# Optimization experiments

Hardware: AMD Instinct MI355X
Metric: run time of the kernel (lower is better)

## Reference

```python
import jax, jax.numpy as jnp
import numpy as np

GAMMA = 20
LAMBDA_INV = 25.0


def setup_inputs() -> dict:
    key = jax.random.key(0)
    k1, k2 = jax.random.split(key)
    B, P, D = 128, 512, 384
    z = jax.random.normal(k1, (B, P, D), dtype=jnp.float32)
    view_ids = jax.random.randint(k2, (P,), 0, 2, dtype=jnp.int64)
    return {"z": z, "view_ids": view_ids}


def reference(z, view_ids):
    B, P, D = z.shape
    # [B, P, P] pairwise similarity per image
    sim = jnp.einsum('bpd,bqd->bpq', z, z)
    # valid pairs: different view and not self
    mask_view = view_ids[None, :] != view_ids[:, None]          # [P, P]
    mask = mask_view & ~jnp.eye(P, dtype=bool)
    sim = jnp.where(mask[None, :, :], sim, jnp.float32(-1.0))
    best_sim = sim.max(axis=2)                                   # [B, P]
    best_j = sim.argmax(axis=2)                                  # [B, P]
    # flatten across batch, global top-gamma anchors
    best_sim_flat = best_sim.reshape(-1)                         # [B*P]
    offsets = jnp.arange(B, dtype=best_j.dtype)[:, None] * P
    best_j_flat = (best_j + offsets).reshape(-1)                 # [B*P]
    topk_vals, topk_idx = jax.lax.top_k(best_sim_flat, GAMMA)
    z_flat = z.reshape(-1, D)
    z1 = z_flat[topk_idx]                                        # anchors
    z2 = z_flat[best_j_flat[topk_idx]]                           # matches
    loss = LAMBDA_INV * jnp.mean((z1 - z2) ** 2)
    fmatch_avg_cos = jax.lax.stop_gradient(topk_vals.mean())
    return loss, fmatch_avg_cos
```

## Files before the change

kernel.cpp:

```cpp
#include <hip/hip_runtime.h>


#define NB 128
#define NP 512
#define ND 384
#define NGAMMA 20
#define NKS 12

typedef __attribute__((ext_vector_type(8))) short short8;
typedef __attribute__((ext_vector_type(4))) float f32x4;

__device__ __forceinline__ unsigned short f2bf(float f) {
    unsigned int u = __float_as_uint(f);
    u += 0x7fffu + ((u >> 16) & 1u);
    return (unsigned short)(u >> 16);
}

__device__ __forceinline__ void gload16(const void* gptr, void* lptr) {
    __builtin_amdgcn_global_load_lds(
        (const __attribute__((address_space(1))) void*)gptr,
        (__attribute__((address_space(3))) void*)lptr, 16, 0, 0);
}

__global__ __launch_bounds__(256) void fm_convert(
    const float* __restrict__ z, unsigned short* __restrict__ zhi)
{
    size_t i = (size_t)blockIdx.x * 256 + threadIdx.x;
    const float4* zp = (const float4*)z + i * 2;
    float4 v0 = zp[0], v1 = zp[1];
    float f[8] = {v0.x, v0.y, v0.z, v0.w, v1.x, v1.y, v1.z, v1.w};
    short8 s;
#pragma unroll
    for (int j = 0; j < 8; ++j) s[j] = (short)f2bf(f[j]);
    *(short8*)&zhi[i * 8] = s;
}

__global__ __launch_bounds__(256, 4) void fm_gemm(
    const unsigned short* __restrict__ zhi, const int* __restrict__ view,
    float* __restrict__ pval, int* __restrict__ pidx)
{
    __shared__ __align__(16) unsigned short Ah[2][4][128][8];
    __shared__ __align__(16) unsigned short Bh[2][4][128][8];
    __shared__ int vs[NP];
    __shared__ float lsv[2][2][64];
    __shared__ int   lsi[2][2][64];
    __shared__ float lqv[2][2][64];
    __shared__ int   lqi[2][2][64];

    const int tid  = threadIdx.x;
    const int lane = tid & 63;
    const int wid  = tid >> 6;
    const int wr   = wid >> 1, wc = wid & 1;
    const int g    = lane >> 4, r = lane & 15;

    const int bid  = blockIdx.x;
    const int gidx = (bid & 7) * 160 + (bid >> 3);
    const int b    = gidx / 10;
    const int t    = gidx % 10;
    int tr, tc;
    if (t < 4)      { tr = 0; tc = t; }
    else if (t < 7) { tr = 1; tc = t - 3; }
    else if (t < 9) { tr = 2; tc = t - 5; }
    else            { tr = 3; tc = 3; }
    const bool diag = (tr == tc);
    const int p0 = tr * 128, q0 = tc * 128;

    vs[tid]       = view[tid];
    vs[tid + 256] = view[tid + 256];
    __builtin_amdgcn_sched_barrier(0);

    const size_t zb = (size_t)b * NP * ND;

    f32x4 acc[4][4];
#pragma unroll
    for (int mi = 0; mi < 4; ++mi)
#pragma unroll
        for (int ni = 0; ni < 4; ++ni) acc[mi][ni] = (f32x4){0.f, 0.f, 0.f, 0.f};

#define STAGE(BUF, KT)                                                           \
    do {                                                                         \
        _Pragma("unroll")                                                        \
        for (int i = 0; i < 2; ++i) {                                            \
            const int c_  = wid * 2 + i;                                         \
            const int kg_ = c_ >> 1;                                             \
            const int rb_ = (c_ & 1) * 64;                                       \
            gload16(zhi + zb + (size_t)(p0 + rb_ + lane) * ND + (KT) * 32 + kg_ * 8, \
                    &Ah[BUF][kg_][rb_][0]);                                      \
            if (!diag)                                                           \
                gload16(zhi + zb + (size_t)(q0 + rb_ + lane) * ND + (KT) * 32 + kg_ * 8, \
                        &Bh[BUF][kg_][rb_][0]);                                  \
        }                                                                        \
    } while (0)

#define COMPUTE(BUF)                                                             \
    do {                                                                         \
        short8 ah_[4], bh_[4];                                                   \
        _Pragma("unroll")                                                        \
        for (int mi = 0; mi < 4; ++mi)                                           \
            ah_[mi] = *(const short8*)&Ah[BUF][g][wr * 64 + mi * 16 + r][0];     \
        _Pragma("unroll")                                                        \
        for (int ni = 0; ni < 4; ++ni)                                           \
            bh_[ni] = diag ? *(const short8*)&Ah[BUF][g][wc * 64 + ni * 16 + r][0] \
                           : *(const short8*)&Bh[BUF][g][wc * 64 + ni * 16 + r][0]; \
        _Pragma("unroll")                                                        \
        for (int mi = 0; mi < 4; ++mi)                                           \
            _Pragma("unroll")                                                    \
            for (int ni = 0; ni < 4; ++ni)                                       \
                acc[mi][ni] = __builtin_amdgcn_mfma_f32_16x16x32_bf16(           \
                    ah_[mi], bh_[ni], acc[mi][ni], 0, 0, 0);                     \
    } while (0)

    STAGE(0, 0);
#pragma unroll
    for (int kt = 0; kt < NKS; ++kt) {
        const int cur = kt & 1;
        __builtin_amdgcn_s_barrier();
        __builtin_amdgcn_sched_barrier(0);
        if (kt + 1 < NKS) {
            STAGE(cur ^ 1, kt + 1);
            if (diag) asm volatile("s_waitcnt vmcnt(2)" ::: "memory");
            else      asm volatile("s_waitcnt vmcnt(4)" ::: "memory");
        } else {
            asm volatile("s_waitcnt vmcnt(0)" ::: "memory");
        }
        __builtin_amdgcn_s_barrier();
        __builtin_amdgcn_sched_barrier(0);
        COMPUTE(cur);
    }
#undef STAGE
#undef COMPUTE

#pragma unroll
    for (int mi = 0; mi < 4; ++mi) {
#pragma unroll
        for (int j = 0; j < 4; ++j) {
            const int prow = p0 + wr * 64 + mi * 16 + g * 4 + j;
            const int rv = vs[prow];
            float bv = -2.0f; int bq = 0;
#pragma unroll
            for (int ni = 0; ni < 4; ++ni) {
                const int q = q0 + wc * 64 + ni * 16 + r;
                const float v = (vs[q] != rv) ? acc[mi][ni][j] : -1.0f;
                if (v > bv) { bv = v; bq = q; }
            }
#pragma unroll
            for (int off = 1; off < 16; off <<= 1) {
                const float ov = __shfl_xor(bv, off);
                const int   oq = __shfl_xor(bq, off);
                if (ov > bv || (ov == bv && oq < bq)) { bv = ov; bq = oq; }
            }
            if (r == 0) {
                lsv[wr][wc][mi * 16 + g * 4 + j] = bv;
                lsi[wr][wc][mi * 16 + g * 4 + j] = bq;
            }
        }
    }
    if (!diag) {
#pragma unroll
        for (int ni = 0; ni < 4; ++ni) {
            const int q = q0 + wc * 64 + ni * 16 + r;
            const int qv = vs[q];
            float bv = -2.0f; int bp = 0;
#pragma unroll
            for (int mi = 0; mi < 4; ++mi)
#pragma unroll
                for (int j = 0; j < 4; ++j) {
                    const int prow = p0 + wr * 64 + mi * 16 + g * 4 + j;
                    const float v = (vs[prow] != qv) ? acc[mi][ni][j] : -1.0f;
                    if (v > bv) { bv = v; bp = prow; }
                }
#pragma unroll
            for (int off = 16; off < 64; off <<= 1) {
                const float ov = __shfl_xor(bv, off);
                const int   op = __shfl_xor(bp, off);
                if (ov > bv || (ov == bv && op < bp)) { bv = ov; bp = op; }
            }
            if (g == 0) {
                lqv[wc][wr][ni * 16 + r] = bv;
                lqi[wc][wr][ni * 16 + r] = bp;
            }
        }
    }
    __syncthreads();
    if (tid < 128) {
        const int half = tid >> 6, row = tid & 63;
        {
            float v0 = lsv[half][0][row]; int i0 = lsi[half][0][row];
            const float v1 = lsv[half][1][row]; const int i1 = lsi[half][1][row];
            if (v1 > v0) { v0 = v1; i0 = i1; }
            const int p = p0 + half * 64 + row;
            pval[((size_t)b * NP + p) * 4 + tc] = v0;
            pidx[((size_t)b * NP + p) * 4 + tc] = i0;
        }
        if (!diag) {
            float v0 = lqv[half][0][row]; int i0 = lqi[half][0][row];
            const float v1 = lqv[half][1][row]; const int i1 = lqi[half][1][row];
            if (v1 > v0) { v0 = v1; i0 = i1; }
            const int q = q0 + half * 64 + row;
            pval[((size_t)b * NP + q) * 4 + tr] = v0;
            pidx[((size_t)b * NP + q) * 4 + tr] = i0;
        }
    }
}

__global__ __launch_bounds__(256) void fm_topk_local(
    const float* __restrict__ pval, float* __restrict__ cval, int* __restrict__ cidx)
{
    __shared__ float sv[1024];
    __shared__ float wv[4];
    __shared__ int   wi[4];

    const int t = threadIdx.x;
    const int base = blockIdx.x * 1024;
#pragma unroll
    for (int i = 0; i < 4; ++i) {
        const int e = t + 256 * i;
        const float4 pv = ((const float4*)pval)[base + e];
        float bv = pv.x;
        if (pv.y > bv) bv = pv.y;
        if (pv.z > bv) bv = pv.z;
        if (pv.w > bv) bv = pv.w;
        sv[e] = bv;
    }
    __syncthreads();

    const int lane = t & 63, w = t >> 6;
    for (int it = 0; it < NGAMMA; ++it) {
        float v = sv[t];
        int pos = t;
#pragma unroll
        for (int i = 1; i < 4; ++i) {
            const int e = t + 256 * i;
            const float x = sv[e];
            if (x > v || (x == v && e < pos)) { v = x; pos = e; }
        }
#pragma unroll
        for (int off = 1; off < 64; off <<= 1) {
            const float ov = __shfl_xor(v, off);
            const int   op = __shfl_xor(pos, off);
            if (ov > v || (ov == v && op < pos)) { v = ov; pos = op; }
        }
        if (lane == 0) { wv[w] = v; wi[w] = pos; }
        __syncthreads();
        if (t == 0) {
            float bv2 = wv[0];
            int bp = wi[0];
            for (int k = 1; k < 4; ++k)
                if (wv[k] > bv2 || (wv[k] == bv2 && wi[k] < bp)) { bv2 = wv[k]; bp = wi[k]; }
            cval[blockIdx.x * NGAMMA + it] = bv2;
            cidx[blockIdx.x * NGAMMA + it] = base + bp;
            sv[bp] = -1e30f;
        }
        __syncthreads();
    }
}

__global__ __launch_bounds__(256) void fm_final(
    const float* __restrict__ cval, const int* __restrict__ cidx,
    const float* __restrict__ pval, const int* __restrict__ pidx,
    const float* __restrict__ z, float* __restrict__ out)
{
    __shared__ float sv[1280];
    __shared__ int   si[1280];
    __shared__ float wv[4];
    __shared__ int   wi[4];
    __shared__ int   sel[NGAMMA];
    __shared__ int   selj[NGAMMA];
    __shared__ float ssum;
    __shared__ float red[4];

    const int t = threadIdx.x;
    for (int e = t; e < 1280; e += 256) { sv[e] = cval[e]; si[e] = cidx[e]; }
    if (t == 0) ssum = 0.f;
    __syncthreads();

    const int lane = t & 63, w = t >> 6;
    for (int it = 0; it < NGAMMA; ++it) {
        float v = sv[t];
        int pos = t;
        for (int e = t + 256; e < 1280; e += 256) {
            const float x = sv[e];
            if (x > v || (x == v && e < pos)) { v = x; pos = e; }
        }
#pragma unroll
        for (int off = 1; off < 64; off <<= 1) {
            const float ov = __shfl_xor(v, off);
            const int   op = __shfl_xor(pos, off);
            if (ov > v || (ov == v && op < pos)) { v = ov; pos = op; }
        }
        if (lane == 0) { wv[w] = v; wi[w] = pos; }
        __syncthreads();
        if (t == 0) {
            float bv2 = wv[0];
            int bp = wi[0];
            for (int k = 1; k < 4; ++k)
                if (wv[k] > bv2 || (wv[k] == bv2 && wi[k] < bp)) { bv2 = wv[k]; bp = wi[k]; }
            sel[it] = si[bp];
            ssum += bv2;
            sv[bp] = -1e30f;
        }
        __syncthreads();
    }

    if (t < NGAMMA) {
        const int a = sel[t];
        const float4 pv = ((const float4*)pval)[a];
        float bv = pv.x; int bc = 0;
        if (pv.y > bv) { bv = pv.y; bc = 1; }
        if (pv.z > bv) { bv = pv.z; bc = 2; }
        if (pv.w > bv) { bv = pv.w; bc = 3; }
        selj[t] = ((a >> 9) << 9) + pidx[(size_t)a * 4 + bc];
    }
    __syncthreads();

    float acc = 0.f;
    for (int pr = 0; pr < NGAMMA; ++pr) {
        const int a = sel[pr];
        const int j = selj[pr];
        const float* za = z + (size_t)a * ND;
        const float* zj = z + (size_t)j * ND;
        for (int d = t; d < ND; d += 256) {
            const float df = za[d] - zj[d];
            acc = fmaf(df, df, acc);
        }
    }
#pragma unroll
    for (int off = 1; off < 64; off <<= 1) acc += __shfl_xor(acc, off);
    if (lane == 0) red[w] = acc;
    __syncthreads();
    if (t == 0) {
        const float tot = red[0] + red[1] + red[2] + red[3];
        out[0] = 25.0f * tot / (float)(NGAMMA * ND);
        out[1] = ssum / (float)NGAMMA;
    }
}

extern "C" void kernel_launch(void* const* d_in, const int* in_sizes, int n_in,
                              void* d_out, int out_size, void* d_ws, size_t ws_size,
                              hipStream_t stream)
{
    const float* z    = (const float*)d_in[0];
    const int*   view = (const int*)d_in[1];
    float*       out  = (float*)d_out;
    char* ws = (char*)d_ws;

    const size_t zhi_off  = 0;
    const size_t pval_off = (size_t)NB * NP * ND * 2;
    const size_t pidx_off = pval_off + (size_t)NB * NP * 4 * 4;
    const size_t cval_off = pidx_off + (size_t)NB * NP * 4 * 4;
    const size_t cidx_off = cval_off + 64 * NGAMMA * 4;

    unsigned short* zhi = (unsigned short*)(ws + zhi_off);
    float* pval = (float*)(ws + pval_off);
    int*   pidx = (int*)(ws + pidx_off);
    float* cval = (float*)(ws + cval_off);
    int*   cidx = (int*)(ws + cidx_off);

    fm_convert<<<(NB * NP * ND) / (8 * 256), 256, 0, stream>>>(z, zhi);
    fm_gemm<<<NB * 10, 256, 0, stream>>>(zhi, view, pval, pidx);
    fm_topk_local<<<(NB * NP) / 1024, 256, 0, stream>>>(pval, cval, cidx);
    fm_final<<<1, 256, 0, stream>>>(cval, cidx, pval, pidx, z, out);
}
```

Baseline: 130.5 us.

## Triple-buffer GEMM loads, drop diag special case, use single-wave top-k kernels

The GEMM moves from a double-buffered to a triple-buffered LDS pipeline with two tiles in flight. It needs only one barrier per k-step, and the epilogue scratch arrays now alias the A buffer to save shared memory. Diagonal tiles now also load B instead of reusing A, which adds redundant global traffic for those tiles. Both top-k kernels become single-wavefront register-resident selections that use no shared memory and no block barriers, cutting per-iteration synchronisation. Occupancy hint drops from 4 to 3 blocks per CU.

Result: slower. 147.4 us (+12.9%).

```diff
diff --git a/kernel.cpp b/kernel.cpp
--- a/kernel.cpp
+++ b/kernel.cpp
@@ -35,17 +35,17 @@
     *(short8*)&zhi[i * 8] = s;
 }
 
-__global__ __launch_bounds__(256, 4) void fm_gemm(
+__global__ __launch_bounds__(256, 3) void fm_gemm(
     const unsigned short* __restrict__ zhi, const int* __restrict__ view,
     float* __restrict__ pval, int* __restrict__ pidx)
 {
-    __shared__ __align__(16) unsigned short Ah[2][4][128][8];
-    __shared__ __align__(16) unsigned short Bh[2][4][128][8];
+    __shared__ __align__(16) unsigned short Ah[3][4][128][8];
+    __shared__ __align__(16) unsigned short Bh[3][4][128][8];
     __shared__ int vs[NP];
-    __shared__ float lsv[2][2][64];
-    __shared__ int   lsi[2][2][64];
-    __shared__ float lqv[2][2][64];
-    __shared__ int   lqi[2][2][64];
+    float* lsv = (float*)&Ah[0][0][0][0];
+    int*   lsi = (int*)lsv + 256;
+    float* lqv = (float*)((int*)lsv + 512);
+    int*   lqi = (int*)lsv + 768;
 
     const int tid  = threadIdx.x;
     const int lane = tid & 63;
@@ -86,9 +86,8 @@
             const int rb_ = (c_ & 1) * 64;                                       \
             gload16(zhi + zb + (size_t)(p0 + rb_ + lane) * ND + (KT) * 32 + kg_ * 8, \
                     &Ah[BUF][kg_][rb_][0]);                                      \
-            if (!diag)                                                           \
-                gload16(zhi + zb + (size_t)(q0 + rb_ + lane) * ND + (KT) * 32 + kg_ * 8, \
-                        &Bh[BUF][kg_][rb_][0]);                                  \
+            gload16(zhi + zb + (size_t)(q0 + rb_ + lane) * ND + (KT) * 32 + kg_ * 8, \
+                    &Bh[BUF][kg_][rb_][0]);                                      \
         }                                                                        \
     } while (0)
 
@@ -100,8 +99,7 @@
             ah_[mi] = *(const short8*)&Ah[BUF][g][wr * 64 + mi * 16 + r][0];     \
         _Pragma("unroll")                                                        \
         for (int ni = 0; ni < 4; ++ni)                                           \
-            bh_[ni] = diag ? *(const short8*)&Ah[BUF][g][wc * 64 + ni * 16 + r][0] \
-                           : *(const short8*)&Bh[BUF][g][wc * 64 + ni * 16 + r][0]; \
+            bh_[ni] = *(const short8*)&Bh[BUF][g][wc * 64 + ni * 16 + r][0];     \
         _Pragma("unroll")                                                        \
         for (int mi = 0; mi < 4; ++mi)                                           \
             _Pragma("unroll")                                                    \
@@ -111,21 +109,16 @@
     } while (0)
 
     STAGE(0, 0);
+    STAGE(1, 1);
 #pragma unroll
     for (int kt = 0; kt < NKS; ++kt) {
-        const int cur = kt & 1;
+        if (kt < NKS - 1) asm volatile("s_waitcnt vmcnt(4)" ::: "memory");
+        else              asm volatile("s_waitcnt vmcnt(0)" ::: "memory");
         __builtin_amdgcn_s_barrier();
         __builtin_amdgcn_sched_barrier(0);
-        if (kt + 1 < NKS) {
-            STAGE(cur ^ 1, kt + 1);
-            if (diag) asm volatile("s_waitcnt vmcnt(2)" ::: "memory");
-            else      asm volatile("s_waitcnt vmcnt(4)" ::: "memory");
-        } else {
-            asm volatile("s_waitcnt vmcnt(0)" ::: "memory");
-        }
-        __builtin_amdgcn_s_barrier();
+        if (kt + 2 < NKS) STAGE((kt + 2) % 3, kt + 2);
         __builtin_amdgcn_sched_barrier(0);
-        COMPUTE(cur);
+        COMPUTE(kt % 3);
     }
 #undef STAGE
 #undef COMPUTE
@@ -150,8 +143,8 @@
                 if (ov > bv || (ov == bv && oq < bq)) { bv = ov; bq = oq; }
             }
             if (r == 0) {
-                lsv[wr][wc][mi * 16 + g * 4 + j] = bv;
-                lsi[wr][wc][mi * 16 + g * 4 + j] = bq;
+                lsv[(wr * 2 + wc) * 64 + mi * 16 + g * 4 + j] = bv;
+                lsi[(wr * 2 + wc) * 64 + mi * 16 + g * 4 + j] = bq;
             }
         }
     }
@@ -176,8 +169,8 @@
                 if (ov > bv || (ov == bv && op < bp)) { bv = ov; bp = op; }
             }
             if (g == 0) {
-                lqv[wc][wr][ni * 16 + r] = bv;
-                lqi[wc][wr][ni * 16 + r] = bp;
+                lqv[(wc * 2 + wr) * 64 + ni * 16 + r] = bv;
+                lqi[(wc * 2 + wr) * 64 + ni * 16 + r] = bp;
             }
         }
     }
@@ -185,16 +178,16 @@
     if (tid < 128) {
         const int half = tid >> 6, row = tid & 63;
         {
-            float v0 = lsv[half][0][row]; int i0 = lsi[half][0][row];
-            const float v1 = lsv[half][1][row]; const int i1 = lsi[half][1][row];
+            float v0 = lsv[(half * 2 + 0) * 64 + row]; int i0 = lsi[(half * 2 + 0) * 64 + row];
+            const float v1 = lsv[(half * 2 + 1) * 64 + row]; const int i1 = lsi[(half * 2 + 1) * 64 + row];
             if (v1 > v0) { v0 = v1; i0 = i1; }
             const int p = p0 + half * 64 + row;
             pval[((size_t)b * NP + p) * 4 + tc] = v0;
             pidx[((size_t)b * NP + p) * 4 + tc] = i0;
         }
         if (!diag) {
-            float v0 = lqv[half][0][row]; int i0 = lqi[half][0][row];
-            const float v1 = lqv[half][1][row]; const int i1 = lqi[half][1][row];
+            float v0 = lqv[(half * 2 + 0) * 64 + row]; int i0 = lqi[(half * 2 + 0) * 64 + row];
+            const float v1 = lqv[(half * 2 + 1) * 64 + row]; const int i1 = lqi[(half * 2 + 1) * 64 + row];
             if (v1 > v0) { v0 = v1; i0 = i1; }
             const int q = q0 + half * 64 + row;
             pval[((size_t)b * NP + q) * 4 + tr] = v0;
@@ -203,55 +196,39 @@
     }
 }
 
-__global__ __launch_bounds__(256) void fm_topk_local(
+__global__ __launch_bounds__(64) void fm_topk_local(
     const float* __restrict__ pval, float* __restrict__ cval, int* __restrict__ cidx)
 {
-    __shared__ float sv[1024];
-    __shared__ float wv[4];
-    __shared__ int   wi[4];
-
-    const int t = threadIdx.x;
+    const int lane = threadIdx.x;
     const int base = blockIdx.x * 1024;
-#pragma unroll
-    for (int i = 0; i < 4; ++i) {
-        const int e = t + 256 * i;
-        const float4 pv = ((const float4*)pval)[base + e];
+    float v[16]; int id[16];
+#pragma unroll
+    for (int i = 0; i < 16; ++i) {
+        const int a = base + i * 64 + lane;
+        const float4 pv = ((const float4*)pval)[a];
         float bv = pv.x;
         if (pv.y > bv) bv = pv.y;
         if (pv.z > bv) bv = pv.z;
         if (pv.w > bv) bv = pv.w;
-        sv[e] = bv;
-    }
-    __syncthreads();
-
-    const int lane = t & 63, w = t >> 6;
+        v[i] = bv; id[i] = a;
+    }
     for (int it = 0; it < NGAMMA; ++it) {
-        float v = sv[t];
-        int pos = t;
-#pragma unroll
-        for (int i = 1; i < 4; ++i) {
-            const int e = t + 256 * i;
-            const float x = sv[e];
-            if (x > v || (x == v && e < pos)) { v = x; pos = e; }
-        }
+        float bv = v[0]; int bi = id[0];
+#pragma unroll
+        for (int i = 1; i < 16; ++i)
+            if (v[i] > bv || (v[i] == bv && id[i] < bi)) { bv = v[i]; bi = id[i]; }
 #pragma unroll
         for (int off = 1; off < 64; off <<= 1) {
-            const float ov = __shfl_xor(v, off);
-            const int   op = __shfl_xor(pos, off);
-            if (ov > v || (ov == v && op < pos)) { v = ov; pos = op; }
-        }
-        if (lane == 0) { wv[w] = v; wi[w] = pos; }
-        __syncthreads();
-        if (t == 0) {
-            float bv2 = wv[0];
-            int bp = wi[0];
-            for (int k = 1; k < 4; ++k)
-                if (wv[k] > bv2 || (wv[k] == bv2 && wi[k] < bp)) { bv2 = wv[k]; bp = wi[k]; }
-            cval[blockIdx.x * NGAMMA + it] = bv2;
-            cidx[blockIdx.x * NGAMMA + it] = base + bp;
-            sv[bp] = -1e30f;
-        }
-        __syncthreads();
+            const float ov = __shfl_xor(bv, off);
+            const int   oi = __shfl_xor(bi, off);
+            if (ov > bv || (ov == bv && oi < bi)) { bv = ov; bi = oi; }
+        }
+        if (lane == 0) {
+            cval[blockIdx.x * NGAMMA + it] = bv;
+            cidx[blockIdx.x * NGAMMA + it] = bi;
+        }
+#pragma unroll
+        for (int i = 0; i < 16; ++i) if (id[i] == bi) v[i] = -1e30f;
     }
 }
 
@@ -260,56 +237,46 @@
     const float* __restrict__ pval, const int* __restrict__ pidx,
     const float* __restrict__ z, float* __restrict__ out)
 {
-    __shared__ float sv[1280];
-    __shared__ int   si[1280];
-    __shared__ float wv[4];
-    __shared__ int   wi[4];
-    __shared__ int   sel[NGAMMA];
-    __shared__ int   selj[NGAMMA];
-    __shared__ float ssum;
+    __shared__ int sel[NGAMMA];
+    __shared__ int selj[NGAMMA];
     __shared__ float red[4];
 
     const int t = threadIdx.x;
-    for (int e = t; e < 1280; e += 256) { sv[e] = cval[e]; si[e] = cidx[e]; }
-    if (t == 0) ssum = 0.f;
-    __syncthreads();
-
     const int lane = t & 63, w = t >> 6;
-    for (int it = 0; it < NGAMMA; ++it) {
-        float v = sv[t];
-        int pos = t;
-        for (int e = t + 256; e < 1280; e += 256) {
-            const float x = sv[e];
-            if (x > v || (x == v && e < pos)) { v = x; pos = e; }
-        }
-#pragma unroll
-        for (int off = 1; off < 64; off <<= 1) {
-            const float ov = __shfl_xor(v, off);
-            const int   op = __shfl_xor(pos, off);
-            if (ov > v || (ov == v && op < pos)) { v = ov; pos = op; }
-        }
-        if (lane == 0) { wv[w] = v; wi[w] = pos; }
-        __syncthreads();
-        if (t == 0) {
-            float bv2 = wv[0];
-            int bp = wi[0];
-            for (int k = 1; k < 4; ++k)
-                if (wv[k] > bv2 || (wv[k] == bv2 && wi[k] < bp)) { bv2 = wv[k]; bp = wi[k]; }
-            sel[it] = si[bp];
-            ssum += bv2;
-            sv[bp] = -1e30f;
-        }
-        __syncthreads();
-    }
-
-    if (t < NGAMMA) {
-        const int a = sel[t];
-        const float4 pv = ((const float4*)pval)[a];
-        float bv = pv.x; int bc = 0;
-        if (pv.y > bv) { bv = pv.y; bc = 1; }
-        if (pv.z > bv) { bv = pv.z; bc = 2; }
-        if (pv.w > bv) { bv = pv.w; bc = 3; }
-        selj[t] = ((a >> 9) << 9) + pidx[(size_t)a * 4 + bc];
+    float ssum = 0.f;
+
+    if (w == 0) {
+        float v[20]; int id[20];
+#pragma unroll
+        for (int i = 0; i < 20; ++i) {
+            const int e = i * 64 + lane;
+            v[i] = cval[e]; id[i] = cidx[e];
+        }
+        for (int it = 0; it < NGAMMA; ++it) {
+            float bv = v[0]; int bi = id[0];
+#pragma unroll
+            for (int i = 1; i < 20; ++i)
+                if (v[i] > bv || (v[i] == bv && id[i] < bi)) { bv = v[i]; bi = id[i]; }
+#pragma unroll
+            for (int off = 1; off < 64; off <<= 1) {
+                const float ov = __shfl_xor(bv, off);
+                const int   oi = __shfl_xor(bi, off);
+                if (ov > bv || (ov == bv && oi < bi)) { bv = ov; bi = oi; }
+            }
+            if (lane == 0) sel[it] = bi;
+            ssum += bv;
+#pragma unroll
+            for (int i = 0; i < 20; ++i) if (id[i] == bi) v[i] = -1e30f;
+        }
+        if (lane < NGAMMA) {
+            const int a = sel[lane];
+            const float4 pv = ((const float4*)pval)[a];
+            float bv = pv.x; int bc = 0;
+            if (pv.y > bv) { bv = pv.y; bc = 1; }
+            if (pv.z > bv) { bv = pv.z; bc = 2; }
+            if (pv.w > bv) { bv = pv.w; bc = 3; }
+            selj[lane] = ((a >> 9) << 9) + pidx[(size_t)a * 4 + bc];
+        }
     }
     __syncthreads();
 
@@ -358,6 +325,6 @@
 
     fm_convert<<<(NB * NP * ND) / (8 * 256), 256, 0, stream>>>(z, zhi);
     fm_gemm<<<NB * 10, 256, 0, stream>>>(zhi, view, pval, pidx);
-    fm_topk_local<<<(NB * NP) / 1024, 256, 0, stream>>>(pval, cval, cidx);
+    fm_topk_local<<<(NB * NP) / 1024, 64, 0, stream>>>(pval, cval, cidx);
     fm_final<<<1, 256, 0, stream>>>(cval, cidx, pval, pidx, z, out);
 }
```
